# Kernel tuning notes

Hardware: AMD Instinct MI355X
Metric: run time of the kernel (lower is better)

The kernel has to match this reference:

```python
import jax, jax.numpy as jnp
import numpy as np


def setup_inputs() -> dict:
    key = jax.random.key(0)
    ks = jax.random.split(key, 7)
    B, N, F, H = 128, 64, 128, 128
    s1 = 1.0 / np.sqrt(2 * N)  # torch Linear default-ish scaling
    s2 = 1.0 / np.sqrt(H)
    return {
        "agent_features": jax.random.normal(ks[0], (B, N, F), dtype=jnp.float32),
        "W1": jax.random.normal(ks[1], (2 * N, H), dtype=jnp.float32) * s1,
        "b1": jax.random.normal(ks[2], (H,), dtype=jnp.float32) * s1,
        "W2": jax.random.normal(ks[3], (H, H), dtype=jnp.float32) * s2,
        "b2": jax.random.normal(ks[4], (H,), dtype=jnp.float32) * s2,
        "w3": jax.random.normal(ks[5], (H,), dtype=jnp.float32) * s2,
        "b3": jax.random.normal(ks[6], (1,), dtype=jnp.float32) * s2,
        "mixing_weights": jnp.ones((N,), dtype=jnp.float32) / N,
    }


def reference(agent_features, W1, b1, W2, b2, w3, b3, mixing_weights):
    N = mixing_weights.shape[0]
    f = agent_features[:, :, :N]  # [B, N, N] (first num_agents features)
    # Split first Linear's weight into the i-half and j-half of the concat:
    # concat([f_i, f_j]) @ W1 == f_i @ W1[:N] + f_j @ W1[N:]
    Ai = jnp.einsum('bnf,fh->bnh', f, W1[:N])   # contribution of agent i
    Aj = jnp.einsum('bnf,fh->bnh', f, W1[N:])   # contribution of agent j
    h1 = jax.nn.relu(Ai[:, :, None, :] + Aj[:, None, :, :] + b1)  # [B,N,N,H]
    h2 = jax.nn.relu(jnp.einsum('bijh,hk->bijk', h1, W2) + b2)    # [B,N,N,H]
    correlations = jax.nn.sigmoid(jnp.einsum('bijh,h->bij', h2, w3) + b3[0])
    weights = jax.nn.softmax(mixing_weights, axis=0)
    return correlations, weights
```

## Files before the change

### kernel.cpp

```cpp
#include <hip/hip_runtime.h>
#include <hip/hip_bf16.h>


typedef __bf16 bf16x8 __attribute__((ext_vector_type(8)));
typedef float f32x4 __attribute__((ext_vector_type(4)));

__global__ __launch_bounds__(512, 4) void fused_kernel(
    const float* __restrict__ af, const float* __restrict__ W1,
    const float* __restrict__ b1, const float* __restrict__ W2,
    const float* __restrict__ b2, const float* __restrict__ w3,
    const float* __restrict__ b3, const float* __restrict__ mw,
    float* __restrict__ out)
{
  __shared__ __align__(16) unsigned short W2s[128 * 128];
  float* const fl = (float*)W2s;
  __shared__ __align__(16) float AjF[64 * 132];
  __shared__ __align__(16) float AiF[16 * 132];
  __shared__ float b2s[128], w3s[128];
  __shared__ float part[2][2][128];

  const int tid  = threadIdx.x;
  const int lane = tid & 63;
  const int wave = tid >> 6;
  const int c = lane & 15, g = lane >> 4;
  const int wm = wave & 1;
  const int wn = wave >> 1;

  const int blk = blockIdx.x;
  const int b   = blk >> 2;
  const int iq  = blk & 3;
  const int ip0 = iq << 3;

  if (blk == 0 && tid < 64) {
    float v = mw[tid];
    float m = v;
    for (int off = 32; off > 0; off >>= 1) m = fmaxf(m, __shfl_xor(m, off));
    float e = expf(v - m);
    float s = e;
    for (int off = 32; off > 0; off >>= 1) s += __shfl_xor(s, off);
    out[128 * 64 * 64 + tid] = e / s;
  }

  {
    const float4* srcQ = (const float4*)(af + (b << 13));
#pragma unroll
    for (int p = 0; p < 2; ++p) {
      const int idx = (p << 9) + tid;
      const int n = idx >> 4, e = idx & 15;
      *(float4*)&fl[(n << 6) + (e << 2)] = srcQ[(n << 5) + e];
    }
    if (tid < 128) b2s[tid] = b2[tid];
    else if (tid < 256) w3s[tid - 128] = w3[tid - 128];
  }

  const int h = tid & 127;
  const int q = tid >> 7;
  const float b1h = b1[h];
  const float bias3 = b3[0];

  __syncthreads();

  {
    float w1c[64];
#pragma unroll
    for (int f = 0; f < 64; ++f) w1c[f] = W1[((64 + f) << 7) + h];
#pragma unroll
    for (int qd = 0; qd < 4; ++qd) {
      const int r0 = (q << 4) + (qd << 2);
      float a0 = 0.f, a1 = 0.f, a2 = 0.f, a3 = 0.f;
#pragma unroll
      for (int fq = 0; fq < 16; ++fq) {
        const float w0  = w1c[fq * 4 + 0];
        const float w1v = w1c[fq * 4 + 1];
        const float w2v = w1c[fq * 4 + 2];
        const float w3v = w1c[fq * 4 + 3];
        const float4 f0 = *(const float4*)&fl[((r0 + 0) << 6) + (fq << 2)];
        const float4 f1 = *(const float4*)&fl[((r0 + 1) << 6) + (fq << 2)];
        const float4 f2 = *(const float4*)&fl[((r0 + 2) << 6) + (fq << 2)];
        const float4 f3 = *(const float4*)&fl[((r0 + 3) << 6) + (fq << 2)];
        a0 = fmaf(f0.x, w0, fmaf(f0.y, w1v, fmaf(f0.z, w2v, fmaf(f0.w, w3v, a0))));
        a1 = fmaf(f1.x, w0, fmaf(f1.y, w1v, fmaf(f1.z, w2v, fmaf(f1.w, w3v, a1))));
        a2 = fmaf(f2.x, w0, fmaf(f2.y, w1v, fmaf(f2.z, w2v, fmaf(f2.w, w3v, a2))));
        a3 = fmaf(f3.x, w0, fmaf(f3.y, w1v, fmaf(f3.z, w2v, fmaf(f3.w, w3v, a3))));
      }
      AjF[(r0 + 0) * 132 + h] = a0;
      AjF[(r0 + 1) * 132 + h] = a1;
      AjF[(r0 + 2) * 132 + h] = a2;
      AjF[(r0 + 3) * 132 + h] = a3;
    }
#pragma unroll
    for (int f = 0; f < 64; ++f) w1c[f] = W1[(f << 7) + h];
    {
      const int r0 = q << 2;
      const int fr = (iq << 4) + r0;
      float a0 = 0.f, a1 = 0.f, a2 = 0.f, a3 = 0.f;
#pragma unroll
      for (int fq = 0; fq < 16; ++fq) {
        const float w0  = w1c[fq * 4 + 0];
        const float w1v = w1c[fq * 4 + 1];
        const float w2v = w1c[fq * 4 + 2];
        const float w3v = w1c[fq * 4 + 3];
        const float4 f0 = *(const float4*)&fl[((fr + 0) << 6) + (fq << 2)];
        const float4 f1 = *(const float4*)&fl[((fr + 1) << 6) + (fq << 2)];
        const float4 f2 = *(const float4*)&fl[((fr + 2) << 6) + (fq << 2)];
        const float4 f3 = *(const float4*)&fl[((fr + 3) << 6) + (fq << 2)];
        a0 = fmaf(f0.x, w0, fmaf(f0.y, w1v, fmaf(f0.z, w2v, fmaf(f0.w, w3v, a0))));
        a1 = fmaf(f1.x, w0, fmaf(f1.y, w1v, fmaf(f1.z, w2v, fmaf(f1.w, w3v, a1))));
        a2 = fmaf(f2.x, w0, fmaf(f2.y, w1v, fmaf(f2.z, w2v, fmaf(f2.w, w3v, a2))));
        a3 = fmaf(f3.x, w0, fmaf(f3.y, w1v, fmaf(f3.z, w2v, fmaf(f3.w, w3v, a3))));
      }
      AiF[(r0 + 0) * 132 + h] = a0 + b1h;
      AiF[(r0 + 1) * 132 + h] = a1 + b1h;
      AiF[(r0 + 2) * 132 + h] = a2 + b1h;
      AiF[(r0 + 3) * 132 + h] = a3 + b1h;
    }
  }

  __syncthreads();

  {
    union U { unsigned short s; __bf16 h; };
    const int ktw = wn;
#pragma unroll
    for (int mt = 0; mt < 4; ++mt) {
      const int m = (wm << 6) + (mt << 4) + c;
      const float* wp = W2 + (((ktw << 5) + (g << 3)) << 7) + m;
      bf16x8 v;
#pragma unroll
      for (int e = 0; e < 8; ++e) {
        unsigned u = __float_as_uint(wp[e << 7]);
        u += 0x7fffu + ((u >> 16) & 1u);
        U cv; cv.s = (unsigned short)(u >> 16);
        v[e] = cv.h;
      }
      *(bf16x8*)&W2s[(m << 7) + ((((ktw << 2) + g) ^ c) << 3)] = v;
    }
  }

  f32x4 ajr[4][2][2];
#pragma unroll
  for (int kt = 0; kt < 4; ++kt)
#pragma unroll
    for (int tn = 0; tn < 2; ++tn) {
      const int j = ((wn << 5) + (tn << 4) + c) & 63;
      const float* ajb = &AjF[j * 132 + (g << 3) + (kt << 5)];
      ajr[kt][tn][0] = *(const f32x4*)(ajb);
      ajr[kt][tn][1] = *(const f32x4*)(ajb + 4);
    }

  __syncthreads();

  const int i_sel = wn >> 1;

  for (int t = 0; t < 8; ++t) {
    const float* aib = &AiF[((t << 1) + i_sel) * 132 + (g << 3)];

    f32x4 acc[4][2];
#pragma unroll
    for (int mt = 0; mt < 4; ++mt) {
      const f32x4 bv = *(const f32x4*)&b2s[(wm << 6) + (mt << 4) + (g << 2)];
      acc[mt][0] = bv;
      acc[mt][1] = bv;
    }

#pragma unroll
    for (int kt = 0; kt < 4; ++kt) {
      const int es = ((kt << 2) + g) ^ c;
      bf16x8 wv[4];
#pragma unroll
      for (int mt = 0; mt < 4; ++mt)
        wv[mt] = *(const bf16x8*)&W2s[(((wm << 6) + (mt << 4) + c) << 7) + (es << 3)];

      const f32x4 a0 = *(const f32x4*)(aib + (kt << 5));
      const f32x4 a1 = *(const f32x4*)(aib + (kt << 5) + 4);
      bf16x8 hv[2];
#pragma unroll
      for (int tn = 0; tn < 2; ++tn) {
        const f32x4 h0  = a0 + ajr[kt][tn][0];
        const f32x4 h1v = a1 + ajr[kt][tn][1];
#pragma unroll
        for (int e = 0; e < 4; ++e) {
          hv[tn][e]     = (__bf16)fmaxf(h0[e], 0.f);
          hv[tn][e + 4] = (__bf16)fmaxf(h1v[e], 0.f);
        }
      }
#pragma unroll
      for (int mt = 0; mt < 4; ++mt)
#pragma unroll
        for (int tn = 0; tn < 2; ++tn)
          acc[mt][tn] = __builtin_amdgcn_mfma_f32_16x16x32_bf16(
              wv[mt], hv[tn], acc[mt][tn], 0, 0, 0);
    }

    float s0 = 0.f, s1 = 0.f;
#pragma unroll
    for (int mt = 0; mt < 4; ++mt) {
      const f32x4 wv3 = *(const f32x4*)&w3s[(wm << 6) + (mt << 4) + (g << 2)];
#pragma unroll
      for (int p = 0; p < 4; ++p) {
        s0 = fmaf(fmaxf(acc[mt][0][p], 0.f), wv3[p], s0);
        s1 = fmaf(fmaxf(acc[mt][1][p], 0.f), wv3[p], s1);
      }
    }
    s0 += __shfl_xor(s0, 16);
    s0 += __shfl_xor(s0, 32);
    s1 += __shfl_xor(s1, 16);
    s1 += __shfl_xor(s1, 32);

    const int pb = t & 1;
    if (g == 0) {
      part[pb][wm][(wn << 5) + c]      = s0;
      part[pb][wm][(wn << 5) + 16 + c] = s1;
    }

    __syncthreads();

    if (tid < 128) {
      const float v = part[pb][0][tid] + part[pb][1][tid] + bias3;
      out[(b << 12) + ((ip0 + t) << 7) + tid] = 1.f / (1.f + __expf(-v));
    }
  }
}

extern "C" void kernel_launch(void* const* d_in, const int* in_sizes, int n_in,
                              void* d_out, int out_size, void* d_ws,
                              size_t ws_size, hipStream_t stream)
{
  const float* af = (const float*)d_in[0];
  const float* W1 = (const float*)d_in[1];
  const float* b1 = (const float*)d_in[2];
  const float* W2 = (const float*)d_in[3];
  const float* b2 = (const float*)d_in[4];
  const float* w3 = (const float*)d_in[5];
  const float* b3 = (const float*)d_in[6];
  const float* mw = (const float*)d_in[7];
  float* out = (float*)d_out;

  (void)d_ws; (void)ws_size;
  fused_kernel<<<512, 512, 0, stream>>>(af, W1, b1, W2, b2, w3, b3, mw, out);
}
```

Baseline: 103.9 us.

## Compute first-layer projections with split-bf16 MFMA instead of scalar FP32 FMAs

The Ai/Aj first-layer projections were computed with per-thread scalar FP32 FMA loops that held 64 W1 values in registers. They now use 16x16x32 bf16 MFMA. Both inputs and W1 are split into high and low bf16 parts, and three MFMAs per K chunk (hi*hi, hi*lo, lo*hi) keep accuracy close to FP32. This lowers VALU work and register pressure in the prologue, at the cost of extra conversion arithmetic and a different shared-memory layout for the staged features.

```diff
diff --git a/kernel.cpp b/kernel.cpp
--- a/kernel.cpp
+++ b/kernel.cpp
@@ -4,6 +4,15 @@
 
 typedef __bf16 bf16x8 __attribute__((ext_vector_type(8)));
 typedef float f32x4 __attribute__((ext_vector_type(4)));
+
+__device__ __forceinline__ unsigned rne16(float x) {
+  unsigned u = __float_as_uint(x);
+  u += 0x7fffu + ((u >> 16) & 1u);
+  return u >> 16;
+}
+__device__ __forceinline__ __bf16 us_as_bf16(unsigned short s) {
+  union { unsigned short s; __bf16 h; } cv; cv.s = s; return cv.h;
+}
 
 __global__ __launch_bounds__(512, 4) void fused_kernel(
     const float* __restrict__ af, const float* __restrict__ W1,
@@ -13,7 +22,8 @@
     float* __restrict__ out)
 {
   __shared__ __align__(16) unsigned short W2s[128 * 128];
-  float* const fl = (float*)W2s;
+  __bf16* const flh = (__bf16*)W2s;
+  __bf16* const fll = flh + 64 * 72;
   __shared__ __align__(16) float AjF[64 * 132];
   __shared__ __align__(16) float AiF[16 * 132];
   __shared__ float b2s[128], w3s[128];
@@ -47,79 +57,79 @@
     for (int p = 0; p < 2; ++p) {
       const int idx = (p << 9) + tid;
       const int n = idx >> 4, e = idx & 15;
-      *(float4*)&fl[(n << 6) + (e << 2)] = srcQ[(n << 5) + e];
+      const float4 v = srcQ[(n << 5) + e];
+      const unsigned h0 = rne16(v.x), h1 = rne16(v.y),
+                     h2 = rne16(v.z), h3 = rne16(v.w);
+      const unsigned l0 = rne16(v.x - __uint_as_float(h0 << 16));
+      const unsigned l1 = rne16(v.y - __uint_as_float(h1 << 16));
+      const unsigned l2 = rne16(v.z - __uint_as_float(h2 << 16));
+      const unsigned l3 = rne16(v.w - __uint_as_float(h3 << 16));
+      uint2 ph; ph.x = h0 | (h1 << 16); ph.y = h2 | (h3 << 16);
+      uint2 pl; pl.x = l0 | (l1 << 16); pl.y = l2 | (l3 << 16);
+      *(uint2*)&flh[n * 72 + (e << 2)] = ph;
+      *(uint2*)&fll[n * 72 + (e << 2)] = pl;
     }
     if (tid < 128) b2s[tid] = b2[tid];
     else if (tid < 256) w3s[tid - 128] = w3[tid - 128];
   }
 
-  const int h = tid & 127;
-  const int q = tid >> 7;
-  const float b1h = b1[h];
   const float bias3 = b3[0];
 
   __syncthreads();
 
   {
-    float w1c[64];
-#pragma unroll
-    for (int f = 0; f < 64; ++f) w1c[f] = W1[((64 + f) << 7) + h];
-#pragma unroll
-    for (int qd = 0; qd < 4; ++qd) {
-      const int r0 = (q << 4) + (qd << 2);
-      float a0 = 0.f, a1 = 0.f, a2 = 0.f, a3 = 0.f;
-#pragma unroll
-      for (int fq = 0; fq < 16; ++fq) {
-        const float w0  = w1c[fq * 4 + 0];
-        const float w1v = w1c[fq * 4 + 1];
-        const float w2v = w1c[fq * 4 + 2];
-        const float w3v = w1c[fq * 4 + 3];
-        const float4 f0 = *(const float4*)&fl[((r0 + 0) << 6) + (fq << 2)];
-        const float4 f1 = *(const float4*)&fl[((r0 + 1) << 6) + (fq << 2)];
-        const float4 f2 = *(const float4*)&fl[((r0 + 2) << 6) + (fq << 2)];
-        const float4 f3 = *(const float4*)&fl[((r0 + 3) << 6) + (fq << 2)];
-        a0 = fmaf(f0.x, w0, fmaf(f0.y, w1v, fmaf(f0.z, w2v, fmaf(f0.w, w3v, a0))));
-        a1 = fmaf(f1.x, w0, fmaf(f1.y, w1v, fmaf(f1.z, w2v, fmaf(f1.w, w3v, a1))));
-        a2 = fmaf(f2.x, w0, fmaf(f2.y, w1v, fmaf(f2.z, w2v, fmaf(f2.w, w3v, a2))));
-        a3 = fmaf(f3.x, w0, fmaf(f3.y, w1v, fmaf(f3.z, w2v, fmaf(f3.w, w3v, a3))));
-      }
-      AjF[(r0 + 0) * 132 + h] = a0;
-      AjF[(r0 + 1) * 132 + h] = a1;
-      AjF[(r0 + 2) * 132 + h] = a2;
-      AjF[(r0 + 3) * 132 + h] = a3;
-    }
-#pragma unroll
-    for (int f = 0; f < 64; ++f) w1c[f] = W1[(f << 7) + h];
+    const int w = wave;
+    bf16x8 ajh[2], ajl[2], aih[2], ail[2];
+#pragma unroll
+    for (int kc = 0; kc < 2; ++kc) {
+      const float* wpj = W1 + ((64 + (kc << 5) + (g << 3)) << 7) + (w << 4) + c;
+      const float* wpi = W1 + (((kc << 5) + (g << 3)) << 7) + (w << 4) + c;
+#pragma unroll
+      for (int e = 0; e < 8; ++e) {
+        const float vj = wpj[e << 7];
+        const unsigned hj = rne16(vj);
+        ajh[kc][e] = us_as_bf16((unsigned short)hj);
+        ajl[kc][e] = us_as_bf16((unsigned short)rne16(vj - __uint_as_float(hj << 16)));
+        const float vi = wpi[e << 7];
+        const unsigned hi_ = rne16(vi);
+        aih[kc][e] = us_as_bf16((unsigned short)hi_);
+        ail[kc][e] = us_as_bf16((unsigned short)rne16(vi - __uint_as_float(hi_ << 16)));
+      }
+    }
+#pragma unroll
+    for (int rt = 0; rt < 4; ++rt) {
+      const __bf16* bp = &flh[((rt << 4) + c) * 72 + (g << 3)];
+      const __bf16* bq = &fll[((rt << 4) + c) * 72 + (g << 3)];
+      f32x4 acc = {0.f, 0.f, 0.f, 0.f};
+#pragma unroll
+      for (int kc = 0; kc < 2; ++kc) {
+        const bf16x8 bh = *(const bf16x8*)(bp + (kc << 5));
+        const bf16x8 bl = *(const bf16x8*)(bq + (kc << 5));
+        acc = __builtin_amdgcn_mfma_f32_16x16x32_bf16(ajh[kc], bh, acc, 0, 0, 0);
+        acc = __builtin_amdgcn_mfma_f32_16x16x32_bf16(ajh[kc], bl, acc, 0, 0, 0);
+        acc = __builtin_amdgcn_mfma_f32_16x16x32_bf16(ajl[kc], bh, acc, 0, 0, 0);
+      }
+      *(f32x4*)&AjF[((rt << 4) + c) * 132 + (w << 4) + (g << 2)] = acc;
+    }
     {
-      const int r0 = q << 2;
-      const int fr = (iq << 4) + r0;
-      float a0 = 0.f, a1 = 0.f, a2 = 0.f, a3 = 0.f;
-#pragma unroll
-      for (int fq = 0; fq < 16; ++fq) {
-        const float w0  = w1c[fq * 4 + 0];
-        const float w1v = w1c[fq * 4 + 1];
-        const float w2v = w1c[fq * 4 + 2];
-        const float w3v = w1c[fq * 4 + 3];
-        const float4 f0 = *(const float4*)&fl[((fr + 0) << 6) + (fq << 2)];
-        const float4 f1 = *(const float4*)&fl[((fr + 1) << 6) + (fq << 2)];
-        const float4 f2 = *(const float4*)&fl[((fr + 2) << 6) + (fq << 2)];
-        const float4 f3 = *(const float4*)&fl[((fr + 3) << 6) + (fq << 2)];
-        a0 = fmaf(f0.x, w0, fmaf(f0.y, w1v, fmaf(f0.z, w2v, fmaf(f0.w, w3v, a0))));
-        a1 = fmaf(f1.x, w0, fmaf(f1.y, w1v, fmaf(f1.z, w2v, fmaf(f1.w, w3v, a1))));
-        a2 = fmaf(f2.x, w0, fmaf(f2.y, w1v, fmaf(f2.z, w2v, fmaf(f2.w, w3v, a2))));
-        a3 = fmaf(f3.x, w0, fmaf(f3.y, w1v, fmaf(f3.z, w2v, fmaf(f3.w, w3v, a3))));
-      }
-      AiF[(r0 + 0) * 132 + h] = a0 + b1h;
-      AiF[(r0 + 1) * 132 + h] = a1 + b1h;
-      AiF[(r0 + 2) * 132 + h] = a2 + b1h;
-      AiF[(r0 + 3) * 132 + h] = a3 + b1h;
+      const __bf16* bp = &flh[((iq << 4) + c) * 72 + (g << 3)];
+      const __bf16* bq = &fll[((iq << 4) + c) * 72 + (g << 3)];
+      f32x4 acc = *(const f32x4*)(b1 + (w << 4) + (g << 2));
+#pragma unroll
+      for (int kc = 0; kc < 2; ++kc) {
+        const bf16x8 bh = *(const bf16x8*)(bp + (kc << 5));
+        const bf16x8 bl = *(const bf16x8*)(bq + (kc << 5));
+        acc = __builtin_amdgcn_mfma_f32_16x16x32_bf16(aih[kc], bh, acc, 0, 0, 0);
+        acc = __builtin_amdgcn_mfma_f32_16x16x32_bf16(aih[kc], bl, acc, 0, 0, 0);
+        acc = __builtin_amdgcn_mfma_f32_16x16x32_bf16(ail[kc], bh, acc, 0, 0, 0);
+      }
+      *(f32x4*)&AiF[c * 132 + (w << 4) + (g << 2)] = acc;
     }
   }
 
   __syncthreads();
 
   {
-    union U { unsigned short s; __bf16 h; };
     const int ktw = wn;
 #pragma unroll
     for (int mt = 0; mt < 4; ++mt) {
@@ -128,10 +138,8 @@
       bf16x8 v;
 #pragma unroll
       for (int e = 0; e < 8; ++e) {
-        unsigned u = __float_as_uint(wp[e << 7]);
-        u += 0x7fffu + ((u >> 16) & 1u);
-        U cv; cv.s = (unsigned short)(u >> 16);
-        v[e] = cv.h;
+        const float vv = wp[e << 7];
+        v[e] = us_as_bf16((unsigned short)rne16(vv));
       }
       *(bf16x8*)&W2s[(m << 7) + ((((ktw << 2) + g) ^ c) << 3)] = v;
     }
```

Measured after the change: 95.32 us (median of 2 runs). -8.3%, faster.
